# Kernel tuning notes

Hardware: AMD Instinct MI355X
Metric: run time of the kernel (lower is better)

## Reference

```python
import jax, jax.numpy as jnp
import numpy as np

EPS = 1e-6        # eigenvalue clamp for numerical safety (matrices are well-conditioned by construction)
MOMENTUM = 0.1    # init kwarg


def _sym_apply(X, fn):
    """Apply a spectral function to a batch of symmetric matrices via eigh."""
    w, V = jnp.linalg.eigh(X)
    w = jnp.maximum(w, EPS)
    return jnp.einsum('...ij,...j,...kj->...ik', V, fn(w), V)


def sqrtm(X):
    return _sym_apply(X, jnp.sqrt)


def invsqrtm(X):
    return _sym_apply(X, lambda w: 1.0 / jnp.sqrt(w))


def logm(X):
    return _sym_apply(X, jnp.log)


def expm_sym(X):
    w, V = jnp.linalg.eigh(X)
    return jnp.einsum('...ij,...j,...kj->...ik', V, jnp.exp(w), V)


def powm(X, t):
    return _sym_apply(X, lambda w: w ** t)


def congr_neg(X, G):
    """CongrG(X, G, 'neg') = G^{-1/2} X G^{-1/2}, broadcast over batch dims of X."""
    Gi = invsqrtm(G)
    return jnp.einsum('ij,...jk,kl->...il', Gi, X, Gi)


def bary_geom(Xm):
    """Karcher (Frechet) mean of SPD matrices Xm: (N, n, n).
    One Karcher-flow step initialized at the arithmetic mean (SPDNet-BN convention)."""
    G = jnp.mean(Xm, axis=0)
    Gs, Gi = sqrtm(G), invsqrtm(G)
    L = logm(jnp.einsum('ij,bjk,kl->bil', Gi, Xm, Gi))   # log-maps at G
    return Gs @ expm_sym(jnp.mean(L, axis=0)) @ Gs


def geodesic(A, B, t):
    """SPD geodesic from A toward B at time t: A^{1/2} (A^{-1/2} B A^{-1/2})^t A^{1/2}."""
    As, Ai = sqrtm(A), invsqrtm(A)
    return As @ powm(Ai @ B @ Ai, t) @ As


def setup_inputs() -> dict:
    key = jax.random.key(0)
    N, T, V, M, n = 32, 64, 25, 2, 16
    A = jax.random.normal(key, (N, T, V, M, n, n), dtype=jnp.float32)
    # SPD construction: A A^T / n + 0.5 I  (min eigenvalue >= 0.5)
    X = jnp.einsum('...ij,...kj->...ik', A, A) / n + 0.5 * jnp.eye(n, dtype=jnp.float32)
    running_mean = jnp.eye(n, dtype=jnp.float32)  # torch.eye(n) in __init__
    return {"X": X, "running_mean": running_mean}


def reference(X, running_mean):
    N, T, V, M, n, _ = X.shape
    Xf = X.reshape(N, T * V * M, n, n)
    X_mean = jnp.mean(Xf, axis=1)                      # (N, n, n) per-sample arithmetic mean
    mean = bary_geom(X_mean)                           # (n, n) Karcher mean over batch
    new_running_mean = geodesic(running_mean, mean, MOMENTUM)  # no_grad EMA in torch
    X_centered = congr_neg(Xf, mean)                   # mean^{-1/2} X mean^{-1/2}
    return X_centered.reshape(N, T, V, M, n, n), new_running_mean
```

## Files before the change

### kernel.cpp

```cpp
#include <hip/hip_runtime.h>
#include <math.h>

#define NS     32
#define BBATCH 3200
#define NMAT   102400
#define EPSC   1e-6f
#define ST     20
#define IX(i,j) ((i)*ST+(j))
#define MSZ    (16*ST)

#define PART_O 0
#define XM_O   131072
#define GS_O   139264
#define GI_O   139520
#define L_O    139776
#define MEAN_O 147968
#define WI_O   148224
#define RS_O   148480
#define RI_O   148736


__device__ __forceinline__ void g2l(const float* __restrict__ g, float* l, int t) {
  if (t < 64) {
    int i = t >> 2, j0 = (t & 3) << 2;
    *(float4*)&l[IX(i, j0)] = *(const float4*)&g[i * 16 + j0];
  }
  __syncthreads();
}

__device__ __forceinline__ void l2g(const float* l, float* __restrict__ g, int t) {
  if (t < 64) {
    int i = t >> 2, j0 = (t & 3) << 2;
    *(float4*)&g[i * 16 + j0] = *(const float4*)&l[IX(i, j0)];
  }
  __syncthreads();
}

__device__ __forceinline__ void mm(const float* A, const float* B, float* C, int t) {
  if (t < 64) {
    int i = t >> 2, j0 = (t & 3) << 2;
    float4 acc = make_float4(0.f, 0.f, 0.f, 0.f);
    #pragma unroll
    for (int k = 0; k < 16; ++k) {
      float a = A[IX(i, k)];
      const float4 b = *(const float4*)&B[IX(k, j0)];
      acc.x += a * b.x; acc.y += a * b.y; acc.z += a * b.z; acc.w += a * b.w;
    }
    *(float4*)&C[IX(i, j0)] = acc;
  }
  __syncthreads();
}

__device__ __forceinline__ void mad_diag(float* C, float s, float d, int t) {
  if (t < 64) {
    int i = t >> 2, j0 = (t & 3) << 2;
    float4 p = *(float4*)&C[IX(i, j0)];
    p.x *= s; p.y *= s; p.z *= s; p.w *= s;
    if (i == j0) p.x += d; else if (i == j0 + 1) p.y += d;
    else if (i == j0 + 2) p.z += d; else if (i == j0 + 3) p.w += d;
    *(float4*)&C[IX(i, j0)] = p;
  }
  __syncthreads();
}

__device__ __forceinline__ void set_scaled_I(float* C, float d, int t) {
  if (t < 64) {
    int i = t >> 2, j0 = (t & 3) << 2;
    float4 p = make_float4(0.f, 0.f, 0.f, 0.f);
    if (i == j0) p.x = d; else if (i == j0 + 1) p.y = d;
    else if (i == j0 + 2) p.z = d; else if (i == j0 + 3) p.w = d;
    *(float4*)&C[IX(i, j0)] = p;
  }
  __syncthreads();
}

__device__ __forceinline__ void symmetrize(float* A, int t) {
  float4 v = make_float4(0.f, 0.f, 0.f, 0.f);
  if (t < 64) {
    int i = t >> 2, j0 = (t & 3) << 2;
    float4 a = *(float4*)&A[IX(i, j0)];
    v.x = 0.5f * (a.x + A[IX(j0,     i)]);
    v.y = 0.5f * (a.y + A[IX(j0 + 1, i)]);
    v.z = 0.5f * (a.z + A[IX(j0 + 2, i)]);
    v.w = 0.5f * (a.w + A[IX(j0 + 3, i)]);
  }
  __syncthreads();
  if (t < 64) {
    int i = t >> 2, j0 = (t & 3) << 2;
    *(float4*)&A[IX(i, j0)] = v;
  }
  __syncthreads();
}

__device__ __forceinline__ float trace16(const float* A) {
  float tr = 0.f;
  #pragma unroll
  for (int k = 0; k < 16; ++k) tr += A[IX(k, k)];
  return tr;
}

#define NS_IT 8
__device__ void ns_sqrtm(const float* A, float* Y0, float* Y1, float* Z0, float* Z1,
                         float* P, int t, float** pS, float** pZ) {
  float c = trace16(A) * (1.f / 16.f);
  float ic = 1.f / c;
  if (t < 64) {
    int i = t >> 2, j0 = (t & 3) << 2;
    float4 a = *(const float4*)&A[IX(i, j0)];
    a.x *= ic; a.y *= ic; a.z *= ic; a.w *= ic;
    *(float4*)&Y0[IX(i, j0)] = a;
    float4 z = make_float4(0.f, 0.f, 0.f, 0.f);
    if (i == j0) z.x = 1.f; else if (i == j0 + 1) z.y = 1.f;
    else if (i == j0 + 2) z.z = 1.f; else if (i == j0 + 3) z.w = 1.f;
    *(float4*)&Z0[IX(i, j0)] = z;
  }
  __syncthreads();
  float *Y = Y0, *Yn = Y1, *Z = Z0, *Zn = Z1;
  for (int it = 0; it < NS_IT; ++it) {
    mm(Z, Y, P, t);
    mad_diag(P, -0.5f, 1.5f, t);
    mm(Y, P, Yn, t);
    mm(P, Z, Zn, t);
    float* tp = Y; Y = Yn; Yn = tp;
    tp = Z; Z = Zn; Zn = tp;
  }
  float sc = sqrtf(c), isc = 1.f / sc;
  if (t < 64) {
    int i = t >> 2, j0 = (t & 3) << 2;
    float4 y = *(float4*)&Y[IX(i, j0)];
    y.x *= sc; y.y *= sc; y.z *= sc; y.w *= sc;
    *(float4*)&Y[IX(i, j0)] = y;
    float4 z = *(float4*)&Z[IX(i, j0)];
    z.x *= isc; z.y *= isc; z.z *= isc; z.w *= isc;
    *(float4*)&Z[IX(i, j0)] = z;
  }
  __syncthreads();
  *pS = Y; *pZ = Z;
}

#define LOG_M 12
__device__ void logm_taylor(float* S, float* L, float* R0, float* R1, int t) {
  mad_diag(S, 1.f, -1.f, t);
  float am = ((LOG_M & 1) ? 1.f : -1.f) / (float)LOG_M;
  set_scaled_I(R0, am, t);
  float *R = R0, *Rn = R1;
  for (int j = LOG_M - 1; j >= 1; --j) {
    mm(S, R, Rn, t);
    float aj = ((j & 1) ? 1.f : -1.f) / (float)j;
    mad_diag(Rn, 1.f, aj, t);
    float* tp = R; R = Rn; Rn = tp;
  }
  mm(S, R, L, t);
}

#define EXP_M 10
__device__ float* expm_taylor(const float* K, float* R0, float* R1, int t) {
  set_scaled_I(R0, 1.f, t);
  float *R = R0, *Rn = R1;
  for (int j = EXP_M; j >= 1; --j) {
    mm(K, R, Rn, t);
    mad_diag(Rn, 1.f / (float)j, 1.f, t);
    float* tp = R; R = Rn; Rn = tp;
  }
  return R;
}


__global__ __launch_bounds__(256) void k_part(const float* __restrict__ X, float* __restrict__ ws) {
  int b = blockIdx.x >> 4;
  int c = blockIdx.x & 15;
  int t = threadIdx.x;
  int e4 = t & 63;
  int r  = t >> 6;
  const float4* X4 = (const float4*)X;
  float4 s = make_float4(0.f, 0.f, 0.f, 0.f);
  long mbase = (long)b * BBATCH + c * 200;
  for (int i = r; i < 200; i += 4) {
    float4 v = X4[(mbase + i) * 64 + e4];
    s.x += v.x; s.y += v.y; s.z += v.z; s.w += v.w;
  }
  __shared__ float4 red[256];
  red[t] = s;
  __syncthreads();
  if (t < 64) {
    float4 a = red[t], b1 = red[t + 64], c1 = red[t + 128], d = red[t + 192];
    float4 o;
    o.x = a.x + b1.x + c1.x + d.x;
    o.y = a.y + b1.y + c1.y + d.y;
    o.z = a.z + b1.z + c1.z + d.z;
    o.w = a.w + b1.w + c1.w + d.w;
    ((float4*)(ws + PART_O))[(long)blockIdx.x * 64 + t] = o;
  }
}

__global__ __launch_bounds__(256) void k_xm(float* __restrict__ ws) {
  int b = blockIdx.x, t = threadIdx.x;
  float a = 0.f;
  for (int c = 0; c < 16; ++c) a += ws[PART_O + (b * 16 + c) * 256 + t];
  ws[XM_O + b * 256 + t] = a * (1.f / BBATCH);
}

__global__ __launch_bounds__(64) void k_prep(const float* __restrict__ rm, float* __restrict__ ws) {
  __shared__ __align__(16) float A[MSZ], Y0[MSZ], Y1[MSZ], Z0[MSZ], Z1[MSZ], P[MSZ];
  int t = threadIdx.x;
  if (blockIdx.x == 0) {
    if (t < 64) {
      int i = t >> 2, j0 = (t & 3) << 2;
      float4 a = make_float4(0.f, 0.f, 0.f, 0.f);
      for (int b = 0; b < NS; ++b) {
        float4 v = *(const float4*)&ws[XM_O + b * 256 + i * 16 + j0];
        a.x += v.x; a.y += v.y; a.z += v.z; a.w += v.w;
      }
      float s = 1.f / NS;
      a.x *= s; a.y *= s; a.z *= s; a.w *= s;
      *(float4*)&A[IX(i, j0)] = a;
    }
    __syncthreads();
  } else {
    g2l(rm, A, t);
  }
  float *S, *Z;
  ns_sqrtm(A, Y0, Y1, Z0, Z1, P, t, &S, &Z);
  l2g(S, ws + (blockIdx.x == 0 ? GS_O : RS_O), t);
  l2g(Z, ws + (blockIdx.x == 0 ? GI_O : RI_O), t);
}

__global__ __launch_bounds__(64) void k_logmap(float* __restrict__ ws) {
  __shared__ __align__(16) float Gi[MSZ], Xb[MSZ], S[MSZ], T[MSZ], R0[MSZ], R1[MSZ];
  int b = blockIdx.x, t = threadIdx.x;
  g2l(ws + GI_O, Gi, t);
  g2l(ws + XM_O + b * 256, Xb, t);
  mm(Gi, Xb, T, t);
  mm(T, Gi, S, t);
  symmetrize(S, t);
  logm_taylor(S, T, R0, R1, t);
  l2g(T, ws + L_O + b * 256, t);
}

__global__ __launch_bounds__(64) void k_mean2(float* __restrict__ ws) {
  __shared__ __align__(16) float K[MSZ], Gs[MSZ], T1[MSZ], T2[MSZ], R0[MSZ], R1[MSZ], P[MSZ];
  int t = threadIdx.x;
  if (t < 64) {
    int i = t >> 2, j0 = (t & 3) << 2;
    float4 a = make_float4(0.f, 0.f, 0.f, 0.f);
    for (int b = 0; b < NS; ++b) {
      float4 v = *(const float4*)&ws[L_O + b * 256 + i * 16 + j0];
      a.x += v.x; a.y += v.y; a.z += v.z; a.w += v.w;
    }
    float s = 1.f / NS;
    a.x *= s; a.y *= s; a.z *= s; a.w *= s;
    *(float4*)&K[IX(i, j0)] = a;
  }
  __syncthreads();
  float* E = expm_taylor(K, R0, R1, t);
  g2l(ws + GS_O, Gs, t);
  mm(Gs, E, T1, t);
  mm(T1, Gs, T2, t);
  symmetrize(T2, t);
  l2g(T2, ws + MEAN_O, t);
  float *S, *Z;
  ns_sqrtm(T2, R0, R1, T1, K, P, t, &S, &Z);
  l2g(Z, ws + WI_O, t);
}

__global__ __launch_bounds__(256) void k_center(const float* __restrict__ X,
                                                const float* __restrict__ ws,
                                                float* __restrict__ out) {
  __shared__ __align__(16) float B0[MSZ], B1[MSZ], B2[MSZ], B3[MSZ], B4[MSZ];
  __shared__ __align__(16) float Xs[4 * MSZ];
  __shared__ __align__(16) float Ts[4 * MSZ];
  __shared__ __align__(16) float Wsm[MSZ];
  int t = threadIdx.x;

  if (blockIdx.x == 0) {
    g2l(ws + RI_O, B0, t);
    g2l(ws + MEAN_O, B1, t);
    mm(B0, B1, B2, t);
    mm(B2, B0, B1, t);
    symmetrize(B1, t);
    float c = trace16(B1) * (1.f / 16.f);
    mad_diag(B1, 1.f / c, 0.f, t);
    logm_taylor(B1, B2, B3, B4, t);
    mad_diag(B2, 0.1f, 0.f, t);
    float* Ep = expm_taylor(B2, B3, B4, t);
    float s = expf(0.1f * logf(c));
    mad_diag(Ep, s, 0.f, t);
    g2l(ws + RS_O, B1, t);
    mm(B1, Ep, B2, t);
    mm(B2, B1, B4, t);
    l2g(B4, out + (size_t)NMAT * 256, t);
  } else {
    long m0 = (long)(blockIdx.x - 1) * 4;
    Wsm[(t >> 4) * ST + (t & 15)] = ws[WI_O + t];
    const float4* X4 = (const float4*)X;
    float4 xv = X4[m0 * 64 + t];
    int mm_ = t >> 6;
    int l  = t & 63;
    int i  = l >> 2;
    int j0 = (l & 3) << 2;
    *(float4*)&Xs[mm_ * MSZ + i * ST + j0] = xv;
    __syncthreads();
    float4 a = make_float4(0.f, 0.f, 0.f, 0.f);
    #pragma unroll
    for (int k = 0; k < 16; ++k) {
      float x = Xs[mm_ * MSZ + i * ST + k];
      const float4 wv = *(const float4*)&Wsm[k * ST + j0];
      a.x += x * wv.x; a.y += x * wv.y; a.z += x * wv.z; a.w += x * wv.w;
    }
    *(float4*)&Ts[mm_ * MSZ + i * ST + j0] = a;
    __syncthreads();
    float4 y = make_float4(0.f, 0.f, 0.f, 0.f);
    #pragma unroll
    for (int k = 0; k < 16; ++k) {
      float w = Wsm[i * ST + k];
      const float4 tv = *(const float4*)&Ts[mm_ * MSZ + k * ST + j0];
      y.x += w * tv.x; y.y += w * tv.y; y.z += w * tv.z; y.w += w * tv.w;
    }
    ((float4*)out)[m0 * 64 + t] = y;
  }
}

extern "C" void kernel_launch(void* const* d_in, const int* in_sizes, int n_in,
                              void* d_out, int out_size, void* d_ws, size_t ws_size,
                              hipStream_t stream) {
  (void)in_sizes; (void)n_in; (void)out_size; (void)ws_size;
  const float* X  = (const float*)d_in[0];
  const float* rm = (const float*)d_in[1];
  float* out = (float*)d_out;
  float* ws  = (float*)d_ws;

  k_part   <<<dim3(512),   dim3(256), 0, stream>>>(X, ws);
  k_xm     <<<dim3(32),    dim3(256), 0, stream>>>(ws);
  k_prep   <<<dim3(2),     dim3(64),  0, stream>>>(rm, ws);
  k_logmap <<<dim3(32),    dim3(64),  0, stream>>>(ws);
  k_mean2  <<<dim3(1),     dim3(64),  0, stream>>>(ws);
  k_center <<<dim3(25601), dim3(256), 0, stream>>>(X, ws, out);
}
```

Measured before the change: 247.9 us.

## Fuse small SPD stages into one block with wave-level sync and fewer iterations

Merges the mean, Newton-Schulz sqrt, log-map, exp and geodesic kernels into a single 1024-thread kernel, where independent matrices are handled by separate wavefronts that synchronise only through LDS waitcnt instead of block barriers. It also cuts the Newton-Schulz, log and exp series lengths, widens the partial-sum reduction blocks, and removes the special geodesic block and one barrier from the centering kernel. The goal is to drop launch overhead and the serial latency of the small-matrix chain. The shorter series may lose accuracy, and relying on waitcnt alone for intra-wave LDS ordering is fragile.

```diff
diff --git a/kernel.cpp b/kernel.cpp
--- a/kernel.cpp
+++ b/kernel.cpp
@@ -1,112 +1,90 @@
 #include <hip/hip_runtime.h>
 #include <math.h>
 
-#define NS     32
+#define NSAMP  32
 #define BBATCH 3200
 #define NMAT   102400
-#define EPSC   1e-6f
 #define ST     20
 #define IX(i,j) ((i)*ST+(j))
 #define MSZ    (16*ST)
 
 #define PART_O 0
-#define XM_O   131072
-#define GS_O   139264
-#define GI_O   139520
-#define L_O    139776
-#define MEAN_O 147968
-#define WI_O   148224
-#define RS_O   148480
-#define RI_O   148736
-
-
-__device__ __forceinline__ void g2l(const float* __restrict__ g, float* l, int t) {
-  if (t < 64) {
-    int i = t >> 2, j0 = (t & 3) << 2;
-    *(float4*)&l[IX(i, j0)] = *(const float4*)&g[i * 16 + j0];
-  }
-  __syncthreads();
-}
-
-__device__ __forceinline__ void l2g(const float* l, float* __restrict__ g, int t) {
-  if (t < 64) {
-    int i = t >> 2, j0 = (t & 3) << 2;
-    *(float4*)&g[i * 16 + j0] = *(const float4*)&l[IX(i, j0)];
-  }
-  __syncthreads();
-}
-
-__device__ __forceinline__ void mm(const float* A, const float* B, float* C, int t) {
-  if (t < 64) {
-    int i = t >> 2, j0 = (t & 3) << 2;
-    float4 acc = make_float4(0.f, 0.f, 0.f, 0.f);
-    #pragma unroll
-    for (int k = 0; k < 16; ++k) {
-      float a = A[IX(i, k)];
-      const float4 b = *(const float4*)&B[IX(k, j0)];
-      acc.x += a * b.x; acc.y += a * b.y; acc.z += a * b.z; acc.w += a * b.w;
-    }
-    *(float4*)&C[IX(i, j0)] = acc;
-  }
-  __syncthreads();
-}
-
-__device__ __forceinline__ void mad_diag(float* C, float s, float d, int t) {
-  if (t < 64) {
-    int i = t >> 2, j0 = (t & 3) << 2;
-    float4 p = *(float4*)&C[IX(i, j0)];
-    p.x *= s; p.y *= s; p.z *= s; p.w *= s;
-    if (i == j0) p.x += d; else if (i == j0 + 1) p.y += d;
-    else if (i == j0 + 2) p.z += d; else if (i == j0 + 3) p.w += d;
-    *(float4*)&C[IX(i, j0)] = p;
-  }
-  __syncthreads();
-}
-
-__device__ __forceinline__ void set_scaled_I(float* C, float d, int t) {
-  if (t < 64) {
-    int i = t >> 2, j0 = (t & 3) << 2;
-    float4 p = make_float4(0.f, 0.f, 0.f, 0.f);
-    if (i == j0) p.x = d; else if (i == j0 + 1) p.y = d;
-    else if (i == j0 + 2) p.z = d; else if (i == j0 + 3) p.w = d;
-    *(float4*)&C[IX(i, j0)] = p;
-  }
-  __syncthreads();
-}
-
-__device__ __forceinline__ void symmetrize(float* A, int t) {
-  float4 v = make_float4(0.f, 0.f, 0.f, 0.f);
-  if (t < 64) {
-    int i = t >> 2, j0 = (t & 3) << 2;
-    float4 a = *(float4*)&A[IX(i, j0)];
-    v.x = 0.5f * (a.x + A[IX(j0,     i)]);
-    v.y = 0.5f * (a.y + A[IX(j0 + 1, i)]);
-    v.z = 0.5f * (a.z + A[IX(j0 + 2, i)]);
-    v.w = 0.5f * (a.w + A[IX(j0 + 3, i)]);
-  }
-  __syncthreads();
-  if (t < 64) {
-    int i = t >> 2, j0 = (t & 3) << 2;
-    *(float4*)&A[IX(i, j0)] = v;
-  }
-  __syncthreads();
-}
-
-__device__ __forceinline__ float trace16(const float* A) {
+#define WI_O   131072
+
+#define NS_IT 5
+#define LOG_M 7
+#define EXP_M 6
+
+
+__device__ __forceinline__ void wsync() {
+  asm volatile("s_waitcnt lgkmcnt(0)" ::: "memory");
+}
+
+__device__ __forceinline__ void wmm(const float* A, const float* B, float* C, int l) {
+  int i = l >> 2, j0 = (l & 3) << 2;
+  float4 acc = make_float4(0.f, 0.f, 0.f, 0.f);
+  #pragma unroll
+  for (int k = 0; k < 16; ++k) {
+    float a = A[IX(i, k)];
+    const float4 b = *(const float4*)&B[IX(k, j0)];
+    acc.x += a * b.x; acc.y += a * b.y; acc.z += a * b.z; acc.w += a * b.w;
+  }
+  *(float4*)&C[IX(i, j0)] = acc;
+  wsync();
+}
+
+__device__ __forceinline__ void wmad_diag(float* C, float s, float d, int l) {
+  int i = l >> 2, j0 = (l & 3) << 2;
+  float4 p = *(float4*)&C[IX(i, j0)];
+  p.x *= s; p.y *= s; p.z *= s; p.w *= s;
+  if (i == j0) p.x += d; else if (i == j0 + 1) p.y += d;
+  else if (i == j0 + 2) p.z += d; else if (i == j0 + 3) p.w += d;
+  *(float4*)&C[IX(i, j0)] = p;
+  wsync();
+}
+
+__device__ __forceinline__ void wset_I(float* C, float d, int l) {
+  int i = l >> 2, j0 = (l & 3) << 2;
+  float4 p = make_float4(0.f, 0.f, 0.f, 0.f);
+  if (i == j0) p.x = d; else if (i == j0 + 1) p.y = d;
+  else if (i == j0 + 2) p.z = d; else if (i == j0 + 3) p.w = d;
+  *(float4*)&C[IX(i, j0)] = p;
+  wsync();
+}
+
+__device__ __forceinline__ void wsym(float* A, int l) {
+  int i = l >> 2, j0 = (l & 3) << 2;
+  float4 a = *(float4*)&A[IX(i, j0)];
+  float4 v;
+  v.x = 0.5f * (a.x + A[IX(j0,     i)]);
+  v.y = 0.5f * (a.y + A[IX(j0 + 1, i)]);
+  v.z = 0.5f * (a.z + A[IX(j0 + 2, i)]);
+  v.w = 0.5f * (a.w + A[IX(j0 + 3, i)]);
+  wsync();
+  *(float4*)&A[IX(i, j0)] = v;
+  wsync();
+}
+
+__device__ __forceinline__ float wtrace(const float* A) {
   float tr = 0.f;
   #pragma unroll
   for (int k = 0; k < 16; ++k) tr += A[IX(k, k)];
   return tr;
 }
 
-#define NS_IT 8
-__device__ void ns_sqrtm(const float* A, float* Y0, float* Y1, float* Z0, float* Z1,
-                         float* P, int t, float** pS, float** pZ) {
-  float c = trace16(A) * (1.f / 16.f);
+__device__ __forceinline__ void wcpy(const float* src, float* dst, int l) {
+  int i = l >> 2, j0 = (l & 3) << 2;
+  *(float4*)&dst[IX(i, j0)] = *(const float4*)&src[IX(i, j0)];
+  wsync();
+}
+
+__device__ void wns(float* Y0, float* Y1, float* Z0, float* Z1, float* P,
+                    int l, float** pS, float** pZ) {
+  float c = wtrace(Y0) * (1.f / 16.f);
   float ic = 1.f / c;
-  if (t < 64) {
-    int i = t >> 2, j0 = (t & 3) << 2;
-    float4 a = *(const float4*)&A[IX(i, j0)];
+  int i = l >> 2, j0 = (l & 3) << 2;
+  {
+    float4 a = *(float4*)&Y0[IX(i, j0)];
     a.x *= ic; a.y *= ic; a.z *= ic; a.w *= ic;
     *(float4*)&Y0[IX(i, j0)] = a;
     float4 z = make_float4(0.f, 0.f, 0.f, 0.f);
@@ -114,19 +92,18 @@
     else if (i == j0 + 2) z.z = 1.f; else if (i == j0 + 3) z.w = 1.f;
     *(float4*)&Z0[IX(i, j0)] = z;
   }
-  __syncthreads();
+  wsync();
   float *Y = Y0, *Yn = Y1, *Z = Z0, *Zn = Z1;
   for (int it = 0; it < NS_IT; ++it) {
-    mm(Z, Y, P, t);
-    mad_diag(P, -0.5f, 1.5f, t);
-    mm(Y, P, Yn, t);
-    mm(P, Z, Zn, t);
+    wmm(Z, Y, P, l);
+    wmad_diag(P, -0.5f, 1.5f, l);
+    wmm(Y, P, Yn, l);
+    wmm(P, Z, Zn, l);
     float* tp = Y; Y = Yn; Yn = tp;
     tp = Z; Z = Zn; Zn = tp;
   }
   float sc = sqrtf(c), isc = 1.f / sc;
-  if (t < 64) {
-    int i = t >> 2, j0 = (t & 3) << 2;
+  {
     float4 y = *(float4*)&Y[IX(i, j0)];
     y.x *= sc; y.y *= sc; y.z *= sc; y.w *= sc;
     *(float4*)&Y[IX(i, j0)] = y;
@@ -134,39 +111,37 @@
     z.x *= isc; z.y *= isc; z.z *= isc; z.w *= isc;
     *(float4*)&Z[IX(i, j0)] = z;
   }
-  __syncthreads();
+  wsync();
   *pS = Y; *pZ = Z;
 }
 
-#define LOG_M 12
-__device__ void logm_taylor(float* S, float* L, float* R0, float* R1, int t) {
-  mad_diag(S, 1.f, -1.f, t);
+__device__ void wlog(float* S, float* L, float* R0, float* R1, int l) {
+  wmad_diag(S, 1.f, -1.f, l);
   float am = ((LOG_M & 1) ? 1.f : -1.f) / (float)LOG_M;
-  set_scaled_I(R0, am, t);
+  wset_I(R0, am, l);
   float *R = R0, *Rn = R1;
   for (int j = LOG_M - 1; j >= 1; --j) {
-    mm(S, R, Rn, t);
+    wmm(S, R, Rn, l);
     float aj = ((j & 1) ? 1.f : -1.f) / (float)j;
-    mad_diag(Rn, 1.f, aj, t);
+    wmad_diag(Rn, 1.f, aj, l);
     float* tp = R; R = Rn; Rn = tp;
   }
-  mm(S, R, L, t);
-}
-
-#define EXP_M 10
-__device__ float* expm_taylor(const float* K, float* R0, float* R1, int t) {
-  set_scaled_I(R0, 1.f, t);
+  wmm(S, R, L, l);
+}
+
+__device__ float* wexp(const float* K, float* R0, float* R1, int l) {
+  wset_I(R0, 1.f, l);
   float *R = R0, *Rn = R1;
   for (int j = EXP_M; j >= 1; --j) {
-    mm(K, R, Rn, t);
-    mad_diag(Rn, 1.f / (float)j, 1.f, t);
+    wmm(K, R, Rn, l);
+    wmad_diag(Rn, 1.f / (float)j, 1.f, l);
     float* tp = R; R = Rn; Rn = tp;
   }
   return R;
 }
 
 
-__global__ __launch_bounds__(256) void k_part(const float* __restrict__ X, float* __restrict__ ws) {
+__global__ __launch_bounds__(512) void k_part(const float* __restrict__ X, float* __restrict__ ws) {
   int b = blockIdx.x >> 4;
   int c = blockIdx.x & 15;
   int t = threadIdx.x;
@@ -175,149 +150,160 @@
   const float4* X4 = (const float4*)X;
   float4 s = make_float4(0.f, 0.f, 0.f, 0.f);
   long mbase = (long)b * BBATCH + c * 200;
-  for (int i = r; i < 200; i += 4) {
+  for (int i = r; i < 200; i += 8) {
     float4 v = X4[(mbase + i) * 64 + e4];
     s.x += v.x; s.y += v.y; s.z += v.z; s.w += v.w;
   }
-  __shared__ float4 red[256];
+  __shared__ float4 red[512];
   red[t] = s;
   __syncthreads();
   if (t < 64) {
-    float4 a = red[t], b1 = red[t + 64], c1 = red[t + 128], d = red[t + 192];
-    float4 o;
-    o.x = a.x + b1.x + c1.x + d.x;
-    o.y = a.y + b1.y + c1.y + d.y;
-    o.z = a.z + b1.z + c1.z + d.z;
-    o.w = a.w + b1.w + c1.w + d.w;
+    float4 o = red[t];
+    #pragma unroll
+    for (int k = 1; k < 8; ++k) {
+      float4 v = red[t + 64 * k];
+      o.x += v.x; o.y += v.y; o.z += v.z; o.w += v.w;
+    }
     ((float4*)(ws + PART_O))[(long)blockIdx.x * 64 + t] = o;
   }
 }
 
-__global__ __launch_bounds__(256) void k_xm(float* __restrict__ ws) {
-  int b = blockIdx.x, t = threadIdx.x;
-  float a = 0.f;
-  for (int c = 0; c < 16; ++c) a += ws[PART_O + (b * 16 + c) * 256 + t];
-  ws[XM_O + b * 256 + t] = a * (1.f / BBATCH);
-}
-
-__global__ __launch_bounds__(64) void k_prep(const float* __restrict__ rm, float* __restrict__ ws) {
-  __shared__ __align__(16) float A[MSZ], Y0[MSZ], Y1[MSZ], Z0[MSZ], Z1[MSZ], P[MSZ];
+__global__ __launch_bounds__(1024) void k_mid(const float* __restrict__ rm,
+                                              float* __restrict__ ws,
+                                              float* __restrict__ out) {
+  __shared__ __align__(16) float XmL[NSAMP * 256];
+  __shared__ __align__(16) float wb[16][4 * MSZ];
+  __shared__ __align__(16) float GsL[MSZ], GiL[MSZ], RsL[MSZ], RiL[MSZ], meanL[MSZ];
   int t = threadIdx.x;
-  if (blockIdx.x == 0) {
-    if (t < 64) {
-      int i = t >> 2, j0 = (t & 3) << 2;
-      float4 a = make_float4(0.f, 0.f, 0.f, 0.f);
-      for (int b = 0; b < NS; ++b) {
-        float4 v = *(const float4*)&ws[XM_O + b * 256 + i * 16 + j0];
-        a.x += v.x; a.y += v.y; a.z += v.z; a.w += v.w;
-      }
-      float s = 1.f / NS;
-      a.x *= s; a.y *= s; a.z *= s; a.w *= s;
-      *(float4*)&A[IX(i, j0)] = a;
+  int w = t >> 6, l = t & 63;
+
+  for (int idx = t; idx < NSAMP * 256; idx += 1024) {
+    int b = idx >> 8, e = idx & 255;
+    float s = 0.f;
+    #pragma unroll
+    for (int c = 0; c < 16; ++c) s += ws[PART_O + (b * 16 + c) * 256 + e];
+    XmL[idx] = s * (1.f / BBATCH);
+  }
+  __syncthreads();
+
+  if (t < 256) {
+    int i = t >> 4, j = t & 15;
+    float s = 0.f;
+    #pragma unroll
+    for (int b = 0; b < NSAMP; ++b) s += XmL[b * 256 + t];
+    wb[0][IX(i, j)] = s * (1.f / NSAMP);
+  } else if (t < 512) {
+    int e = t - 256, i = e >> 4, j = e & 15;
+    wb[1][IX(i, j)] = rm[e];
+  }
+  __syncthreads();
+
+  if (w == 0) {
+    float *S, *Z;
+    wns(&wb[0][0], &wb[0][MSZ], &wb[0][2*MSZ], &wb[0][3*MSZ], &wb[2][0], l, &S, &Z);
+    wcpy(S, GsL, l); wcpy(Z, GiL, l);
+  } else if (w == 1) {
+    float *S, *Z;
+    wns(&wb[1][0], &wb[1][MSZ], &wb[1][2*MSZ], &wb[1][3*MSZ], &wb[3][0], l, &S, &Z);
+    wcpy(S, RsL, l); wcpy(Z, RiL, l);
+  }
+  __syncthreads();
+
+  {
+    float* B0 = &wb[w][0];       float* B1 = &wb[w][MSZ];
+    float* B2 = &wb[w][2 * MSZ]; float* B3 = &wb[w][3 * MSZ];
+    int i = l >> 2, j0 = (l & 3) << 2;
+    for (int r = 0; r < 2; ++r) {
+      int b = w + r * 16;
+      *(float4*)&B0[IX(i, j0)] = *(const float4*)&XmL[b * 256 + i * 16 + j0];
+      wsync();
+      wmm(GiL, B0, B1, l);
+      wmm(B1, GiL, B2, l);
+      wsym(B2, l);
+      wlog(B2, B3, B0, B1, l);
+      *(float4*)&XmL[b * 256 + i * 16 + j0] = *(const float4*)&B3[IX(i, j0)];
+      wsync();
     }
-    __syncthreads();
-  } else {
-    g2l(rm, A, t);
-  }
-  float *S, *Z;
-  ns_sqrtm(A, Y0, Y1, Z0, Z1, P, t, &S, &Z);
-  l2g(S, ws + (blockIdx.x == 0 ? GS_O : RS_O), t);
-  l2g(Z, ws + (blockIdx.x == 0 ? GI_O : RI_O), t);
-}
-
-__global__ __launch_bounds__(64) void k_logmap(float* __restrict__ ws) {
-  __shared__ __align__(16) float Gi[MSZ], Xb[MSZ], S[MSZ], T[MSZ], R0[MSZ], R1[MSZ];
-  int b = blockIdx.x, t = threadIdx.x;
-  g2l(ws + GI_O, Gi, t);
-  g2l(ws + XM_O + b * 256, Xb, t);
-  mm(Gi, Xb, T, t);
-  mm(T, Gi, S, t);
-  symmetrize(S, t);
-  logm_taylor(S, T, R0, R1, t);
-  l2g(T, ws + L_O + b * 256, t);
-}
-
-__global__ __launch_bounds__(64) void k_mean2(float* __restrict__ ws) {
-  __shared__ __align__(16) float K[MSZ], Gs[MSZ], T1[MSZ], T2[MSZ], R0[MSZ], R1[MSZ], P[MSZ];
-  int t = threadIdx.x;
-  if (t < 64) {
-    int i = t >> 2, j0 = (t & 3) << 2;
-    float4 a = make_float4(0.f, 0.f, 0.f, 0.f);
-    for (int b = 0; b < NS; ++b) {
-      float4 v = *(const float4*)&ws[L_O + b * 256 + i * 16 + j0];
-      a.x += v.x; a.y += v.y; a.z += v.z; a.w += v.w;
-    }
-    float s = 1.f / NS;
-    a.x *= s; a.y *= s; a.z *= s; a.w *= s;
-    *(float4*)&K[IX(i, j0)] = a;
-  }
-  __syncthreads();
-  float* E = expm_taylor(K, R0, R1, t);
-  g2l(ws + GS_O, Gs, t);
-  mm(Gs, E, T1, t);
-  mm(T1, Gs, T2, t);
-  symmetrize(T2, t);
-  l2g(T2, ws + MEAN_O, t);
-  float *S, *Z;
-  ns_sqrtm(T2, R0, R1, T1, K, P, t, &S, &Z);
-  l2g(Z, ws + WI_O, t);
+  }
+  __syncthreads();
+
+  if (t < 256) {
+    int i = t >> 4, j = t & 15;
+    float s = 0.f;
+    #pragma unroll
+    for (int b = 0; b < NSAMP; ++b) s += XmL[b * 256 + t];
+    wb[0][IX(i, j)] = s * (1.f / NSAMP);
+  }
+  __syncthreads();
+  if (w == 0) {
+    float* E = wexp(&wb[0][0], &wb[0][MSZ], &wb[0][2 * MSZ], l);
+    wmm(GsL, E, &wb[0][3 * MSZ], l);
+    wmm(&wb[0][3 * MSZ], GsL, &wb[0][0], l);
+    wsym(&wb[0][0], l);
+    wcpy(&wb[0][0], meanL, l);
+  }
+  __syncthreads();
+
+  if (w == 0) {
+    wcpy(meanL, &wb[0][0], l);
+    float *S, *Z;
+    wns(&wb[0][0], &wb[0][MSZ], &wb[0][2*MSZ], &wb[0][3*MSZ], &wb[2][0], l, &S, &Z);
+    int i = l >> 2, j0 = (l & 3) << 2;
+    *(float4*)&ws[WI_O + i * 16 + j0] = *(const float4*)&Z[IX(i, j0)];
+  } else if (w == 1) {
+    float* b0 = &wb[1][0];       float* b1 = &wb[1][MSZ];
+    float* b2 = &wb[1][2 * MSZ]; float* b3 = &wb[1][3 * MSZ];
+    wmm(RiL, meanL, b0, l);
+    wmm(b0, RiL, b1, l);
+    wsym(b1, l);
+    float c = wtrace(b1) * (1.f / 16.f);
+    wmad_diag(b1, 1.f / c, 0.f, l);
+    wlog(b1, b2, b0, b3, l);
+    wmad_diag(b2, 0.1f, 0.f, l);
+    float* E = wexp(b2, b0, b3, l);
+    float s = expf(0.1f * logf(c));
+    wmad_diag(E, s, 0.f, l);
+    wmm(RsL, E, b1, l);
+    wmm(b1, RsL, b3, l);
+    int i = l >> 2, j0 = (l & 3) << 2;
+    *(float4*)&out[(size_t)NMAT * 256 + i * 16 + j0] = *(const float4*)&b3[IX(i, j0)];
+  }
 }
 
 __global__ __launch_bounds__(256) void k_center(const float* __restrict__ X,
                                                 const float* __restrict__ ws,
                                                 float* __restrict__ out) {
-  __shared__ __align__(16) float B0[MSZ], B1[MSZ], B2[MSZ], B3[MSZ], B4[MSZ];
+  __shared__ __align__(16) float Wsm[MSZ];
   __shared__ __align__(16) float Xs[4 * MSZ];
   __shared__ __align__(16) float Ts[4 * MSZ];
-  __shared__ __align__(16) float Wsm[MSZ];
   int t = threadIdx.x;
-
-  if (blockIdx.x == 0) {
-    g2l(ws + RI_O, B0, t);
-    g2l(ws + MEAN_O, B1, t);
-    mm(B0, B1, B2, t);
-    mm(B2, B0, B1, t);
-    symmetrize(B1, t);
-    float c = trace16(B1) * (1.f / 16.f);
-    mad_diag(B1, 1.f / c, 0.f, t);
-    logm_taylor(B1, B2, B3, B4, t);
-    mad_diag(B2, 0.1f, 0.f, t);
-    float* Ep = expm_taylor(B2, B3, B4, t);
-    float s = expf(0.1f * logf(c));
-    mad_diag(Ep, s, 0.f, t);
-    g2l(ws + RS_O, B1, t);
-    mm(B1, Ep, B2, t);
-    mm(B2, B1, B4, t);
-    l2g(B4, out + (size_t)NMAT * 256, t);
-  } else {
-    long m0 = (long)(blockIdx.x - 1) * 4;
-    Wsm[(t >> 4) * ST + (t & 15)] = ws[WI_O + t];
-    const float4* X4 = (const float4*)X;
-    float4 xv = X4[m0 * 64 + t];
-    int mm_ = t >> 6;
-    int l  = t & 63;
-    int i  = l >> 2;
-    int j0 = (l & 3) << 2;
-    *(float4*)&Xs[mm_ * MSZ + i * ST + j0] = xv;
-    __syncthreads();
-    float4 a = make_float4(0.f, 0.f, 0.f, 0.f);
-    #pragma unroll
-    for (int k = 0; k < 16; ++k) {
-      float x = Xs[mm_ * MSZ + i * ST + k];
-      const float4 wv = *(const float4*)&Wsm[k * ST + j0];
-      a.x += x * wv.x; a.y += x * wv.y; a.z += x * wv.z; a.w += x * wv.w;
-    }
-    *(float4*)&Ts[mm_ * MSZ + i * ST + j0] = a;
-    __syncthreads();
-    float4 y = make_float4(0.f, 0.f, 0.f, 0.f);
-    #pragma unroll
-    for (int k = 0; k < 16; ++k) {
-      float w = Wsm[i * ST + k];
-      const float4 tv = *(const float4*)&Ts[mm_ * MSZ + k * ST + j0];
-      y.x += w * tv.x; y.y += w * tv.y; y.z += w * tv.z; y.w += w * tv.w;
-    }
-    ((float4*)out)[m0 * 64 + t] = y;
-  }
+  long m0 = (long)blockIdx.x * 4;
+  Wsm[(t >> 4) * ST + (t & 15)] = ws[WI_O + t];
+  const float4* X4 = (const float4*)X;
+  float4 xv = X4[m0 * 64 + t];
+  int mw = t >> 6;
+  int l  = t & 63;
+  int i  = l >> 2;
+  int j0 = (l & 3) << 2;
+  *(float4*)&Xs[mw * MSZ + i * ST + j0] = xv;
+  __syncthreads();
+  float4 a = make_float4(0.f, 0.f, 0.f, 0.f);
+  #pragma unroll
+  for (int k = 0; k < 16; ++k) {
+    float x = Xs[mw * MSZ + i * ST + k];
+    const float4 wv = *(const float4*)&Wsm[k * ST + j0];
+    a.x += x * wv.x; a.y += x * wv.y; a.z += x * wv.z; a.w += x * wv.w;
+  }
+  *(float4*)&Ts[mw * MSZ + i * ST + j0] = a;
+  wsync();
+  float4 y = make_float4(0.f, 0.f, 0.f, 0.f);
+  #pragma unroll
+  for (int k = 0; k < 16; ++k) {
+    float w = Wsm[i * ST + k];
+    const float4 tv = *(const float4*)&Ts[mw * MSZ + k * ST + j0];
+    y.x += w * tv.x; y.y += w * tv.y; y.z += w * tv.z; y.w += w * tv.w;
+  }
+  ((float4*)out)[m0 * 64 + t] = y;
 }
 
 extern "C" void kernel_launch(void* const* d_in, const int* in_sizes, int n_in,
@@ -329,10 +315,7 @@
   float* out = (float*)d_out;
   float* ws  = (float*)d_ws;
 
-  k_part   <<<dim3(512),   dim3(256), 0, stream>>>(X, ws);
-  k_xm     <<<dim3(32),    dim3(256), 0, stream>>>(ws);
-  k_prep   <<<dim3(2),     dim3(64),  0, stream>>>(rm, ws);
-  k_logmap <<<dim3(32),    dim3(64),  0, stream>>>(ws);
-  k_mean2  <<<dim3(1),     dim3(64),  0, stream>>>(ws);
-  k_center <<<dim3(25601), dim3(256), 0, stream>>>(X, ws, out);
-}
+  k_part   <<<dim3(512),   dim3(512),  0, stream>>>(X, ws);
+  k_mid    <<<dim3(1),     dim3(1024), 0, stream>>>(rm, ws, out);
+  k_center <<<dim3(25600), dim3(256),  0, stream>>>(X, ws, out);
+}
```

Result: no change. 247.4 us (-0.2%).
